# Kernel tuning notes

Hardware: AMD Instinct MI355X
Metric: run time of the kernel (lower is better)

Reference implementation:

```python
import jax, jax.numpy as jnp
import numpy as np

B = 32768      # batch size
D = 256        # embedding dim
C = 2048       # number of classes (label range)
WEIGHT = 1.0
TEMPERATURE = 0.3
EPS = 1e-12


def setup_inputs() -> dict:
    key = jax.random.key(0)
    k1, k2 = jax.random.split(key)
    features = jax.random.normal(k1, (B, D), dtype=jnp.float32)
    labels = jax.random.randint(k2, (B,), 0, C, dtype=jnp.int32)
    return {"features": features, "labels": labels, "epoch": 5}


def reference(features, labels, epoch):
    # L2-normalize embeddings (F.normalize, p=2, dim=1)
    norms = jnp.sqrt(jnp.sum(features * features, axis=1, keepdims=True))
    f = features / jnp.maximum(norms, EPS)                      # [B, D]

    # per-class segment sums / counts (vectorized replacement of the python loop)
    ones = jnp.ones((f.shape[0],), dtype=f.dtype)
    counts = jax.ops.segment_sum(ones, labels, num_segments=C)  # [C]
    sums = jax.ops.segment_sum(f, labels, num_segments=C)       # [C, D]
    centroids = sums / jnp.maximum(counts, 1.0)[:, None]        # [C, D] (mean; empty classes masked later)

    # leave-one-out positive centroid: (sum_class - f_i) / (n_class - 1)
    cnt_i = counts[labels]                                       # [B]
    c_p = (sums[labels] - f) / jnp.maximum(cnt_i - 1.0, 1.0)[:, None]
    d_p = jnp.sqrt(jnp.sum((f - c_p) ** 2, axis=1) + EPS)        # [B]

    # distances to all class centroids: ||f||=1 after normalization
    cn2 = jnp.sum(centroids * centroids, axis=1)                 # [C]
    d2 = 1.0 + cn2[None, :] - 2.0 * (f @ centroids.T)           # [B, C]
    d = jnp.sqrt(jnp.maximum(d2, EPS))

    # mask own class and empty (absent-in-batch) classes, take min negative distance
    class_ids = jnp.arange(C, dtype=labels.dtype)
    neg_mask = (counts[None, :] > 0) & (labels[:, None] != class_ids[None, :])
    d_n = jnp.min(jnp.where(neg_mask, d, jnp.inf), axis=1)       # [B]

    # samples are skipped if their class is a singleton or no negative class exists
    valid = (cnt_i > 1.0) & jnp.isfinite(d_n)
    d_n_safe = jnp.where(jnp.isfinite(d_n), d_n, 0.0)

    # temperature schedule: min(temperature + 0.02*epoch, 1)
    temp = min(TEMPERATURE + 0.02 * epoch, 1.0)

    # ln(1 + exp((d_p - d_n)/t)) == softplus
    loss_per_sample = jax.nn.softplus((d_p - d_n_safe) / temp)
    cnt = jnp.sum(valid.astype(f.dtype))
    loss = jnp.where(cnt > 0,
                     jnp.sum(jnp.where(valid, loss_per_sample, 0.0)) / jnp.maximum(cnt, 1.0),
                     0.0)
    return WEIGHT * loss
```

## Files before the change

### kernel.cpp

```cpp
#include <hip/hip_runtime.h>
#include <hip/hip_bf16.h>
#include <math.h>

constexpr int Bn = 32768;
constexpr int Dn = 256;
constexpr int Cn = 2048;
constexpr int NSPLIT = 4;
constexpr int CLS_PER_BLK = Cn / NSPLIT;
constexpr int TCLS = 32;
constexpr int NIT = CLS_PER_BLK / TCLS;
#define EPSF 1e-12f
#define INFF __builtin_inff()

typedef __bf16 bf16x8 __attribute__((ext_vector_type(8)));
typedef __bf16 bf16x4 __attribute__((ext_vector_type(4)));
typedef float  f32x4  __attribute__((ext_vector_type(4)));

__device__ inline void async_copy16(const void* g, void* l) {
    __builtin_amdgcn_global_load_lds(
        (const __attribute__((address_space(1))) void*)g,
        (__attribute__((address_space(3))) void*)l, 16, 0, 0);
}

__global__ __launch_bounds__(256) void k_prep(const float* __restrict__ feat,
                                              const int* __restrict__ labels,
                                              __bf16* __restrict__ fneg,
                                              int* __restrict__ hist) {
    const int wave = threadIdx.x >> 6, lane = threadIdx.x & 63;
    const int s = blockIdx.x * 4 + wave;
    const float4 v = ((const float4*)(feat + (size_t)s * Dn))[lane];
    float ss = v.x * v.x + v.y * v.y + v.z * v.z + v.w * v.w;
    #pragma unroll
    for (int off = 1; off < 64; off <<= 1) ss += __shfl_xor(ss, off, 64);
    const float inv = -2.0f / fmaxf(sqrtf(ss), EPSF);
    bf16x4 bf;
    bf[0] = (__bf16)(v.x * inv); bf[1] = (__bf16)(v.y * inv);
    bf[2] = (__bf16)(v.z * inv); bf[3] = (__bf16)(v.w * inv);
    *(bf16x4*)(fneg + (size_t)s * Dn + lane * 4) = bf;
    if (lane == 0) atomicAdd(&hist[labels[s]], 1);
}

__global__ __launch_bounds__(256) void k_scan(const int* __restrict__ hist,
                                              int* __restrict__ cnt_i,
                                              int* __restrict__ offs,
                                              int* __restrict__ offs_work) {
    __shared__ int part[256];
    const int t = threadIdx.x;
    int h[8], pre[8]; int sum = 0;
    #pragma unroll
    for (int j = 0; j < 8; ++j) { h[j] = hist[t * 8 + j]; pre[j] = sum; sum += h[j]; }
    int v = sum;
    part[t] = v; __syncthreads();
    for (int off = 1; off < 256; off <<= 1) {
        int add = (t >= off) ? part[t - off] : 0;
        __syncthreads();
        v += add; part[t] = v;
        __syncthreads();
    }
    const int base = v - sum;
    #pragma unroll
    for (int j = 0; j < 8; ++j) {
        const int b = t * 8 + j, o = base + pre[j];
        cnt_i[b] = h[j]; offs[b] = o; offs_work[b] = o;
    }
}

__global__ __launch_bounds__(256) void k_scatter(const int* __restrict__ labels,
                                                 int* __restrict__ offs_work,
                                                 int* __restrict__ order) {
    const int i = blockIdx.x * 256 + threadIdx.x;
    const int pos = atomicAdd(&offs_work[labels[i]], 1);
    order[pos] = i;
}

__global__ __launch_bounds__(256) void k_centseg(const __bf16* __restrict__ fneg,
                                                 const int* __restrict__ order,
                                                 const int* __restrict__ offs,
                                                 const int* __restrict__ cnt_i,
                                                 __bf16* __restrict__ centK,
                                                 float* __restrict__ cn2x) {
    const int wave = threadIdx.x >> 6, lane = threadIdx.x & 63;
    const int c = blockIdx.x * 4 + wave;
    const int n = cnt_i[c], start = offs[c];
    int myidx = 0;
    if (lane < n) myidx = order[start + lane];
    float sx = 0.f, sy = 0.f, sz = 0.f, sw = 0.f;
    const int nf = (n < 64) ? n : 64;
    for (int j = 0; j < nf; ++j) {
        const int idx = __shfl(myidx, j, 64);
        const bf16x4 v = *(const bf16x4*)(fneg + (size_t)idx * Dn + lane * 4);
        sx += -0.5f * (float)v[0]; sy += -0.5f * (float)v[1];
        sz += -0.5f * (float)v[2]; sw += -0.5f * (float)v[3];
    }
    for (int j = 64; j < n; ++j) {
        const int idx = order[start + j];
        const bf16x4 v = *(const bf16x4*)(fneg + (size_t)idx * Dn + lane * 4);
        sx += -0.5f * (float)v[0]; sy += -0.5f * (float)v[1];
        sz += -0.5f * (float)v[2]; sw += -0.5f * (float)v[3];
    }
    const float invn = 1.0f / fmaxf((float)n, 1.0f);
    const float cx = sx * invn, cy = sy * invn, cz = sz * invn, cw = sw * invn;
    bf16x4 cb; cb[0] = (__bf16)cx; cb[1] = (__bf16)cy; cb[2] = (__bf16)cz; cb[3] = (__bf16)cw;
    *(bf16x4*)(centK + ((size_t)(lane >> 1) * Cn + c) * 8 + (lane & 1) * 4) = cb;
    float ss = cx * cx + cy * cy + cz * cz + cw * cw;
    #pragma unroll
    for (int off = 1; off < 64; off <<= 1) ss += __shfl_xor(ss, off, 64);
    if (lane == 0) cn2x[c] = (n > 0) ? ss : INFF;
}

__global__ __launch_bounds__(256, 2) void k_main(const __bf16* __restrict__ fneg,
                                                 const int* __restrict__ labels,
                                                 const __bf16* __restrict__ centK,
                                                 const float* __restrict__ cn2x,
                                                 float* __restrict__ minval,
                                                 float* __restrict__ dotown) {
    __shared__ __align__(16) __bf16 sB[2][TCLS * Dn];
    __shared__ float s_cn2[CLS_PER_BLK];
    const int lane = threadIdx.x & 63, wave = threadIdx.x >> 6;
    const int m16 = lane & 15, quad = lane >> 4;
    const int sbase = blockIdx.x * 256 + wave * 64;
    const int c_begin = blockIdx.y * CLS_PER_BLK;

    bf16x8 a[4][8];
    #pragma unroll
    for (int p = 0; p < 4; ++p) {
        const __bf16* fr = fneg + (size_t)(sbase + p * 16 + m16) * Dn + quad * 8;
        #pragma unroll
        for (int t = 0; t < 8; ++t) a[p][t] = *(const bf16x8*)(fr + t * 32);
    }
    int lab[4][4];
    #pragma unroll
    for (int p = 0; p < 4; ++p)
        #pragma unroll
        for (int r = 0; r < 4; ++r)
            lab[p][r] = labels[sbase + p * 16 + quad * 4 + r];

    float rm[4][4], dacc[4][4];
    #pragma unroll
    for (int p = 0; p < 4; ++p)
        #pragma unroll
        for (int r = 0; r < 4; ++r) { rm[p][r] = INFF; dacc[p][r] = 0.0f; }

    auto stage = [&](int buf, int it) {
        const int c0 = c_begin + it * TCLS;
        #pragma unroll
        for (int j = 0; j < 4; ++j) {
            const int chunk = wave * 256 + j * 64 + lane;
            const int h  = chunk >> 9;
            const int kc = (chunk >> 4) & 31;
            const int n  = chunk & 15;
            const __bf16* g = centK + ((size_t)kc * Cn + (c0 + h * 16 + n)) * 8;
            __bf16* l = &sB[buf][(size_t)(wave * 256 + j * 64) * 8];
            async_copy16(g, l);
        }
    };

    stage(0, 0);
    for (int c = threadIdx.x; c < CLS_PER_BLK; c += 256) s_cn2[c] = cn2x[c_begin + c];
    __syncthreads();
    for (int it = 0; it < NIT; ++it) {
        const int cur = it & 1;
        if (it + 1 < NIT) stage(cur ^ 1, it + 1);
        #pragma unroll
        for (int hh = 0; hh < 2; ++hh) {
            const int ctile = it * TCLS + hh * 16;
            const float cn2v = s_cn2[ctile + m16];
            const __bf16* ls = &sB[cur][hh * 4096];
            f32x4 acc[4] = {{0.f,0.f,0.f,0.f},{0.f,0.f,0.f,0.f},
                            {0.f,0.f,0.f,0.f},{0.f,0.f,0.f,0.f}};
            #pragma unroll
            for (int t = 0; t < 8; ++t) {
                const bf16x8 b = *(const bf16x8*)(ls + t * 512 + lane * 8);
                #pragma unroll
                for (int p = 0; p < 4; ++p)
                    acc[p] = __builtin_amdgcn_mfma_f32_16x16x32_bf16(a[p][t], b, acc[p], 0, 0, 0);
            }
            const int crow = c_begin + ctile + m16;
            #pragma unroll
            for (int p = 0; p < 4; ++p)
                #pragma unroll
                for (int r = 0; r < 4; ++r) {
                    const bool own = (crow == lab[p][r]);
                    const float sel = own ? INFF : cn2v;
                    rm[p][r] = fminf(rm[p][r], sel + acc[p][r]);
                    dacc[p][r] += own ? acc[p][r] : 0.0f;
                }
        }
        __syncthreads();
    }
    #pragma unroll
    for (int off = 1; off < 16; off <<= 1)
        #pragma unroll
        for (int p = 0; p < 4; ++p)
            #pragma unroll
            for (int r = 0; r < 4; ++r) {
                rm[p][r] = fminf(rm[p][r], __shfl_xor(rm[p][r], off, 64));
                dacc[p][r] += __shfl_xor(dacc[p][r], off, 64);
            }
    if (m16 == 0) {
        float* mv = minval + (size_t)blockIdx.y * Bn;
        float* dv = dotown + (size_t)blockIdx.y * Bn;
        #pragma unroll
        for (int p = 0; p < 4; ++p)
            #pragma unroll
            for (int r = 0; r < 4; ++r) {
                mv[sbase + p * 16 + quad * 4 + r] = rm[p][r];
                dv[sbase + p * 16 + quad * 4 + r] = dacc[p][r];
            }
    }
}

__global__ __launch_bounds__(256) void k_final(const int* __restrict__ labels,
                                               const int* __restrict__ cnt_i,
                                               const float* __restrict__ cn2x,
                                               const float* __restrict__ minval,
                                               const float* __restrict__ dotown,
                                               const int* __restrict__ epoch,
                                               float* __restrict__ accum) {
    const int i = blockIdx.x * 256 + threadIdx.x;
    const int lane = threadIdx.x & 63;
    const float temp = fminf(0.3f + 0.02f * (float)(*epoch), 1.0f);
    float m = minval[i];
    float draw = dotown[i];
    #pragma unroll
    for (int k = 1; k < NSPLIT; ++k) {
        m = fminf(m, minval[(size_t)k * Bn + i]);
        draw += dotown[(size_t)k * Bn + i];
    }
    const int l = labels[i];
    const int n = cnt_i[l];
    const float nf = (float)n;
    const float cn2 = cn2x[l];
    const float fds = nf * (-0.5f * draw);
    const float fm1 = fmaxf(nf - 1.0f, 1.0f);
    const float fdcp = (fds - 1.0f) / fm1;
    const float cp2 = (nf * nf * cn2 - 2.0f * fds + 1.0f) / (fm1 * fm1);
    const float dp2 = 1.0f - 2.0f * fdcp + cp2;
    const float d_p = sqrtf(fmaxf(dp2, 0.0f) + EPSF);
    const bool finite = (m < 1e37f);
    const float d_n = finite ? sqrtf(fmaxf(1.0f + m, EPSF)) : 0.0f;
    const bool valid = (n > 1) && finite;
    const float x = (d_p - d_n) / temp;
    const float sp = fmaxf(x, 0.0f) + log1pf(expf(-fabsf(x)));
    float ws = valid ? sp : 0.0f, wc = valid ? 1.0f : 0.0f;
    #pragma unroll
    for (int off = 1; off < 64; off <<= 1) {
        ws += __shfl_xor(ws, off, 64);
        wc += __shfl_xor(wc, off, 64);
    }
    if (lane == 0) {
        atomicAdd(&accum[0], ws);
        atomicAdd(&accum[1], wc);
    }
}

__global__ void k_out(const float* __restrict__ accum, float* __restrict__ out) {
    const float s = accum[0], c = accum[1];
    out[0] = (c > 0.0f) ? (s / fmaxf(c, 1.0f)) : 0.0f;
}

extern "C" void kernel_launch(void* const* d_in, const int* in_sizes, int n_in,
                              void* d_out, int out_size, void* d_ws, size_t ws_size,
                              hipStream_t stream) {
    const float* feat  = (const float*)d_in[0];
    const int* labels  = (const int*)d_in[1];
    const int* epoch   = (const int*)d_in[2];
    float* out = (float*)d_out;
    char* ws = (char*)d_ws;

    size_t off = 0;
    __bf16* fneg     = (__bf16*)(ws + off); off += (size_t)Bn * Dn * 2;
    __bf16* centK    = (__bf16*)(ws + off); off += (size_t)Cn * Dn * 2;
    float*  cn2x     = (float*)(ws + off);  off += (size_t)Cn * 4;
    int*    hist     = (int*)(ws + off);    off += (size_t)Cn * 4;
    int*    cnt_i    = (int*)(ws + off);    off += (size_t)Cn * 4;
    int*    offs     = (int*)(ws + off);    off += (size_t)Cn * 4;
    int*    offs_wk  = (int*)(ws + off);    off += (size_t)Cn * 4;
    int*    order    = (int*)(ws + off);    off += (size_t)Bn * 4;
    float*  minval   = (float*)(ws + off);  off += (size_t)NSPLIT * Bn * 4;
    float*  dotown   = (float*)(ws + off);  off += (size_t)NSPLIT * Bn * 4;
    float*  accum    = (float*)(ws + off);  off += 2 * 4;

    (void)hipMemsetAsync(hist,  0, (size_t)Cn * sizeof(int), stream);
    (void)hipMemsetAsync(accum, 0, 2 * sizeof(float), stream);

    k_prep<<<Bn / 4, 256, 0, stream>>>(feat, labels, fneg, hist);
    k_scan<<<1, 256, 0, stream>>>(hist, cnt_i, offs, offs_wk);
    k_scatter<<<Bn / 256, 256, 0, stream>>>(labels, offs_wk, order);
    k_centseg<<<Cn / 4, 256, 0, stream>>>(fneg, order, offs, cnt_i, centK, cn2x);
    dim3 g5(Bn / 256, NSPLIT);
    k_main<<<g5, 256, 0, stream>>>(fneg, labels, centK, cn2x, minval, dotown);
    k_final<<<Bn / 256, 256, 0, stream>>>(labels, cnt_i, cn2x, minval, dotown,
                                          epoch, accum);
    k_out<<<1, 1, 0, stream>>>(accum, out);
}
```

Baseline: 162.5 us.

## Fuse all stages into one persistent kernel with software grid barriers

Replaces the seven separate kernel launches and two memsets with a single persistent kernel of 512 blocks. Stages are separated by an atomic-counter grid barrier, and the three zeroed buffers are laid out contiguously so one memset clears them. The aim is to remove launch gaps and per-kernel tail effects. In exchange it adds six global barriers, relies on all 512 blocks being co-resident (256 CUs times 2 blocks), and has a bounded spin guard that could silently break the barrier. Stages that used many small blocks now run on fewer blocks with more work each.

```diff
diff --git a/kernel.cpp b/kernel.cpp
--- a/kernel.cpp
+++ b/kernel.cpp
@@ -9,6 +9,7 @@
 constexpr int CLS_PER_BLK = Cn / NSPLIT;
 constexpr int TCLS = 32;
 constexpr int NIT = CLS_PER_BLK / TCLS;
+constexpr int NBLK = 512;
 #define EPSF 1e-12f
 #define INFF __builtin_inff()
 
@@ -22,241 +23,259 @@
         (__attribute__((address_space(3))) void*)l, 16, 0, 0);
 }
 
-__global__ __launch_bounds__(256) void k_prep(const float* __restrict__ feat,
-                                              const int* __restrict__ labels,
-                                              __bf16* __restrict__ fneg,
-                                              int* __restrict__ hist) {
-    const int wave = threadIdx.x >> 6, lane = threadIdx.x & 63;
-    const int s = blockIdx.x * 4 + wave;
-    const float4 v = ((const float4*)(feat + (size_t)s * Dn))[lane];
-    float ss = v.x * v.x + v.y * v.y + v.z * v.z + v.w * v.w;
-    #pragma unroll
-    for (int off = 1; off < 64; off <<= 1) ss += __shfl_xor(ss, off, 64);
-    const float inv = -2.0f / fmaxf(sqrtf(ss), EPSF);
-    bf16x4 bf;
-    bf[0] = (__bf16)(v.x * inv); bf[1] = (__bf16)(v.y * inv);
-    bf[2] = (__bf16)(v.z * inv); bf[3] = (__bf16)(v.w * inv);
-    *(bf16x4*)(fneg + (size_t)s * Dn + lane * 4) = bf;
-    if (lane == 0) atomicAdd(&hist[labels[s]], 1);
+__device__ inline void gbar(unsigned* bar, unsigned target) {
+    __syncthreads();
+    if (threadIdx.x == 0) {
+        __threadfence();
+        __hip_atomic_fetch_add(bar, 1u, __ATOMIC_RELAXED, __HIP_MEMORY_SCOPE_AGENT);
+        int guard = 0;
+        while (__hip_atomic_load(bar, __ATOMIC_RELAXED, __HIP_MEMORY_SCOPE_AGENT) < target
+               && guard < (1 << 22)) {
+            __builtin_amdgcn_s_sleep(2);
+            ++guard;
+        }
+        __threadfence();
+    }
+    __syncthreads();
 }
 
-__global__ __launch_bounds__(256) void k_scan(const int* __restrict__ hist,
-                                              int* __restrict__ cnt_i,
-                                              int* __restrict__ offs,
-                                              int* __restrict__ offs_work) {
-    __shared__ int part[256];
-    const int t = threadIdx.x;
-    int h[8], pre[8]; int sum = 0;
-    #pragma unroll
-    for (int j = 0; j < 8; ++j) { h[j] = hist[t * 8 + j]; pre[j] = sum; sum += h[j]; }
-    int v = sum;
-    part[t] = v; __syncthreads();
-    for (int off = 1; off < 256; off <<= 1) {
-        int add = (t >= off) ? part[t - off] : 0;
-        __syncthreads();
-        v += add; part[t] = v;
-        __syncthreads();
-    }
-    const int base = v - sum;
-    #pragma unroll
-    for (int j = 0; j < 8; ++j) {
-        const int b = t * 8 + j, o = base + pre[j];
-        cnt_i[b] = h[j]; offs[b] = o; offs_work[b] = o;
-    }
-}
-
-__global__ __launch_bounds__(256) void k_scatter(const int* __restrict__ labels,
-                                                 int* __restrict__ offs_work,
-                                                 int* __restrict__ order) {
-    const int i = blockIdx.x * 256 + threadIdx.x;
-    const int pos = atomicAdd(&offs_work[labels[i]], 1);
-    order[pos] = i;
-}
-
-__global__ __launch_bounds__(256) void k_centseg(const __bf16* __restrict__ fneg,
-                                                 const int* __restrict__ order,
-                                                 const int* __restrict__ offs,
-                                                 const int* __restrict__ cnt_i,
-                                                 __bf16* __restrict__ centK,
-                                                 float* __restrict__ cn2x) {
-    const int wave = threadIdx.x >> 6, lane = threadIdx.x & 63;
-    const int c = blockIdx.x * 4 + wave;
-    const int n = cnt_i[c], start = offs[c];
-    int myidx = 0;
-    if (lane < n) myidx = order[start + lane];
-    float sx = 0.f, sy = 0.f, sz = 0.f, sw = 0.f;
-    const int nf = (n < 64) ? n : 64;
-    for (int j = 0; j < nf; ++j) {
-        const int idx = __shfl(myidx, j, 64);
-        const bf16x4 v = *(const bf16x4*)(fneg + (size_t)idx * Dn + lane * 4);
-        sx += -0.5f * (float)v[0]; sy += -0.5f * (float)v[1];
-        sz += -0.5f * (float)v[2]; sw += -0.5f * (float)v[3];
-    }
-    for (int j = 64; j < n; ++j) {
-        const int idx = order[start + j];
-        const bf16x4 v = *(const bf16x4*)(fneg + (size_t)idx * Dn + lane * 4);
-        sx += -0.5f * (float)v[0]; sy += -0.5f * (float)v[1];
-        sz += -0.5f * (float)v[2]; sw += -0.5f * (float)v[3];
-    }
-    const float invn = 1.0f / fmaxf((float)n, 1.0f);
-    const float cx = sx * invn, cy = sy * invn, cz = sz * invn, cw = sw * invn;
-    bf16x4 cb; cb[0] = (__bf16)cx; cb[1] = (__bf16)cy; cb[2] = (__bf16)cz; cb[3] = (__bf16)cw;
-    *(bf16x4*)(centK + ((size_t)(lane >> 1) * Cn + c) * 8 + (lane & 1) * 4) = cb;
-    float ss = cx * cx + cy * cy + cz * cz + cw * cw;
-    #pragma unroll
-    for (int off = 1; off < 64; off <<= 1) ss += __shfl_xor(ss, off, 64);
-    if (lane == 0) cn2x[c] = (n > 0) ? ss : INFF;
-}
-
-__global__ __launch_bounds__(256, 2) void k_main(const __bf16* __restrict__ fneg,
-                                                 const int* __restrict__ labels,
-                                                 const __bf16* __restrict__ centK,
-                                                 const float* __restrict__ cn2x,
-                                                 float* __restrict__ minval,
-                                                 float* __restrict__ dotown) {
+__global__ __launch_bounds__(256, 2) void k_all(
+    const float* __restrict__ feat, const int* __restrict__ labels,
+    const int* __restrict__ epoch,
+    __bf16* __restrict__ fneg, __bf16* __restrict__ centK,
+    float* __restrict__ cn2x, int* __restrict__ hist,
+    int* __restrict__ cnt_i, int* __restrict__ offs,
+    int* __restrict__ offs_wk, int* __restrict__ order,
+    float* __restrict__ minval, float* __restrict__ dotown,
+    float* __restrict__ accum, unsigned* __restrict__ bar,
+    float* __restrict__ out)
+{
+    const int tid = threadIdx.x, bx = blockIdx.x;
+    const int lane = tid & 63, wave = tid >> 6;
+
     __shared__ __align__(16) __bf16 sB[2][TCLS * Dn];
     __shared__ float s_cn2[CLS_PER_BLK];
-    const int lane = threadIdx.x & 63, wave = threadIdx.x >> 6;
-    const int m16 = lane & 15, quad = lane >> 4;
-    const int sbase = blockIdx.x * 256 + wave * 64;
-    const int c_begin = blockIdx.y * CLS_PER_BLK;
-
-    bf16x8 a[4][8];
-    #pragma unroll
-    for (int p = 0; p < 4; ++p) {
-        const __bf16* fr = fneg + (size_t)(sbase + p * 16 + m16) * Dn + quad * 8;
-        #pragma unroll
-        for (int t = 0; t < 8; ++t) a[p][t] = *(const bf16x8*)(fr + t * 32);
-    }
-    int lab[4][4];
-    #pragma unroll
-    for (int p = 0; p < 4; ++p)
-        #pragma unroll
-        for (int r = 0; r < 4; ++r)
-            lab[p][r] = labels[sbase + p * 16 + quad * 4 + r];
-
-    float rm[4][4], dacc[4][4];
-    #pragma unroll
-    for (int p = 0; p < 4; ++p)
-        #pragma unroll
-        for (int r = 0; r < 4; ++r) { rm[p][r] = INFF; dacc[p][r] = 0.0f; }
-
-    auto stage = [&](int buf, int it) {
-        const int c0 = c_begin + it * TCLS;
-        #pragma unroll
-        for (int j = 0; j < 4; ++j) {
-            const int chunk = wave * 256 + j * 64 + lane;
-            const int h  = chunk >> 9;
-            const int kc = (chunk >> 4) & 31;
-            const int n  = chunk & 15;
-            const __bf16* g = centK + ((size_t)kc * Cn + (c0 + h * 16 + n)) * 8;
-            __bf16* l = &sB[buf][(size_t)(wave * 256 + j * 64) * 8];
-            async_copy16(g, l);
-        }
-    };
-
-    stage(0, 0);
-    for (int c = threadIdx.x; c < CLS_PER_BLK; c += 256) s_cn2[c] = cn2x[c_begin + c];
-    __syncthreads();
-    for (int it = 0; it < NIT; ++it) {
-        const int cur = it & 1;
-        if (it + 1 < NIT) stage(cur ^ 1, it + 1);
-        #pragma unroll
-        for (int hh = 0; hh < 2; ++hh) {
-            const int ctile = it * TCLS + hh * 16;
-            const float cn2v = s_cn2[ctile + m16];
-            const __bf16* ls = &sB[cur][hh * 4096];
-            f32x4 acc[4] = {{0.f,0.f,0.f,0.f},{0.f,0.f,0.f,0.f},
-                            {0.f,0.f,0.f,0.f},{0.f,0.f,0.f,0.f}};
-            #pragma unroll
-            for (int t = 0; t < 8; ++t) {
-                const bf16x8 b = *(const bf16x8*)(ls + t * 512 + lane * 8);
+
+    {
+        #pragma unroll 4
+        for (int w = 0; w < 16; ++w) {
+            const int s = bx * 64 + w * 4 + wave;
+            const float4 v = ((const float4*)(feat + (size_t)s * Dn))[lane];
+            float ss = v.x * v.x + v.y * v.y + v.z * v.z + v.w * v.w;
+            #pragma unroll
+            for (int off = 1; off < 64; off <<= 1) ss += __shfl_xor(ss, off, 64);
+            const float inv = -2.0f / fmaxf(sqrtf(ss), EPSF);
+            bf16x4 bf;
+            bf[0] = (__bf16)(v.x * inv); bf[1] = (__bf16)(v.y * inv);
+            bf[2] = (__bf16)(v.z * inv); bf[3] = (__bf16)(v.w * inv);
+            *(bf16x4*)(fneg + (size_t)s * Dn + lane * 4) = bf;
+            if (lane == 0) atomicAdd(&hist[labels[s]], 1);
+        }
+    }
+    gbar(bar, 1u * NBLK);
+
+    if (bx == 0) {
+        int* part = (int*)s_cn2;
+        int h[8], pre[8]; int sum = 0;
+        #pragma unroll
+        for (int j = 0; j < 8; ++j) { h[j] = hist[tid * 8 + j]; pre[j] = sum; sum += h[j]; }
+        int v = sum;
+        part[tid] = v; __syncthreads();
+        for (int off = 1; off < 256; off <<= 1) {
+            int add = (tid >= off) ? part[tid - off] : 0;
+            __syncthreads();
+            v += add; part[tid] = v;
+            __syncthreads();
+        }
+        const int base = v - sum;
+        #pragma unroll
+        for (int j = 0; j < 8; ++j) {
+            const int b = tid * 8 + j, o = base + pre[j];
+            cnt_i[b] = h[j]; offs[b] = o; offs_wk[b] = o;
+        }
+    }
+    gbar(bar, 2u * NBLK);
+
+    {
+        const int i = bx * 256 + tid;
+        if (i < Bn) {
+            const int pos = atomicAdd(&offs_wk[labels[i]], 1);
+            order[pos] = i;
+        }
+    }
+    gbar(bar, 3u * NBLK);
+
+    {
+        const int c = bx * 4 + wave;
+        const int n = cnt_i[c], start = offs[c];
+        int myidx = 0;
+        if (lane < n) myidx = order[start + lane];
+        float sx = 0.f, sy = 0.f, sz = 0.f, sw = 0.f;
+        const int nf = (n < 64) ? n : 64;
+        for (int j = 0; j < nf; ++j) {
+            const int idx = __shfl(myidx, j, 64);
+            const bf16x4 v = *(const bf16x4*)(fneg + (size_t)idx * Dn + lane * 4);
+            sx += -0.5f * (float)v[0]; sy += -0.5f * (float)v[1];
+            sz += -0.5f * (float)v[2]; sw += -0.5f * (float)v[3];
+        }
+        for (int j = 64; j < n; ++j) {
+            const int idx = order[start + j];
+            const bf16x4 v = *(const bf16x4*)(fneg + (size_t)idx * Dn + lane * 4);
+            sx += -0.5f * (float)v[0]; sy += -0.5f * (float)v[1];
+            sz += -0.5f * (float)v[2]; sw += -0.5f * (float)v[3];
+        }
+        const float invn = 1.0f / fmaxf((float)n, 1.0f);
+        const float cx = sx * invn, cy = sy * invn, cz = sz * invn, cw = sw * invn;
+        bf16x4 cb; cb[0] = (__bf16)cx; cb[1] = (__bf16)cy;
+        cb[2] = (__bf16)cz; cb[3] = (__bf16)cw;
+        *(bf16x4*)(centK + ((size_t)(lane >> 1) * Cn + c) * 8 + (lane & 1) * 4) = cb;
+        float ss = cx * cx + cy * cy + cz * cz + cw * cw;
+        #pragma unroll
+        for (int off = 1; off < 64; off <<= 1) ss += __shfl_xor(ss, off, 64);
+        if (lane == 0) cn2x[c] = (n > 0) ? ss : INFF;
+    }
+    gbar(bar, 4u * NBLK);
+
+    {
+        const int bxm = bx & 127, split = bx >> 7;
+        const int m16 = lane & 15, quad = lane >> 4;
+        const int sbase = bxm * 256 + wave * 64;
+        const int c_begin = split * CLS_PER_BLK;
+
+        bf16x8 a[4][8];
+        #pragma unroll
+        for (int p = 0; p < 4; ++p) {
+            const __bf16* fr = fneg + (size_t)(sbase + p * 16 + m16) * Dn + quad * 8;
+            #pragma unroll
+            for (int t = 0; t < 8; ++t) a[p][t] = *(const bf16x8*)(fr + t * 32);
+        }
+        int lab[4][4];
+        #pragma unroll
+        for (int p = 0; p < 4; ++p)
+            #pragma unroll
+            for (int r = 0; r < 4; ++r)
+                lab[p][r] = labels[sbase + p * 16 + quad * 4 + r];
+
+        float rm[4][4], dacc[4][4];
+        #pragma unroll
+        for (int p = 0; p < 4; ++p)
+            #pragma unroll
+            for (int r = 0; r < 4; ++r) { rm[p][r] = INFF; dacc[p][r] = 0.0f; }
+
+        auto stage = [&](int buf, int it) {
+            const int c0 = c_begin + it * TCLS;
+            #pragma unroll
+            for (int j = 0; j < 4; ++j) {
+                const int chunk = wave * 256 + j * 64 + lane;
+                const int h  = chunk >> 9;
+                const int kc = (chunk >> 4) & 31;
+                const int n  = chunk & 15;
+                const __bf16* g = centK + ((size_t)kc * Cn + (c0 + h * 16 + n)) * 8;
+                __bf16* l = &sB[buf][(size_t)(wave * 256 + j * 64) * 8];
+                async_copy16(g, l);
+            }
+        };
+
+        stage(0, 0);
+        for (int c = tid; c < CLS_PER_BLK; c += 256) s_cn2[c] = cn2x[c_begin + c];
+        __syncthreads();
+        for (int it = 0; it < NIT; ++it) {
+            const int cur = it & 1;
+            if (it + 1 < NIT) stage(cur ^ 1, it + 1);
+            #pragma unroll
+            for (int hh = 0; hh < 2; ++hh) {
+                const int ctile = it * TCLS + hh * 16;
+                const float cn2v = s_cn2[ctile + m16];
+                const __bf16* ls = &sB[cur][hh * 4096];
+                f32x4 acc[4] = {{0.f,0.f,0.f,0.f},{0.f,0.f,0.f,0.f},
+                                {0.f,0.f,0.f,0.f},{0.f,0.f,0.f,0.f}};
+                #pragma unroll
+                for (int t = 0; t < 8; ++t) {
+                    const bf16x8 b = *(const bf16x8*)(ls + t * 512 + lane * 8);
+                    #pragma unroll
+                    for (int p = 0; p < 4; ++p)
+                        acc[p] = __builtin_amdgcn_mfma_f32_16x16x32_bf16(a[p][t], b, acc[p], 0, 0, 0);
+                }
+                const int crow = c_begin + ctile + m16;
                 #pragma unroll
                 for (int p = 0; p < 4; ++p)
-                    acc[p] = __builtin_amdgcn_mfma_f32_16x16x32_bf16(a[p][t], b, acc[p], 0, 0, 0);
-            }
-            const int crow = c_begin + ctile + m16;
+                    #pragma unroll
+                    for (int r = 0; r < 4; ++r) {
+                        const bool own = (crow == lab[p][r]);
+                        const float sel = own ? INFF : cn2v;
+                        rm[p][r] = fminf(rm[p][r], sel + acc[p][r]);
+                        dacc[p][r] += own ? acc[p][r] : 0.0f;
+                    }
+            }
+            __syncthreads();
+        }
+        #pragma unroll
+        for (int off = 1; off < 16; off <<= 1)
             #pragma unroll
             for (int p = 0; p < 4; ++p)
                 #pragma unroll
                 for (int r = 0; r < 4; ++r) {
-                    const bool own = (crow == lab[p][r]);
-                    const float sel = own ? INFF : cn2v;
-                    rm[p][r] = fminf(rm[p][r], sel + acc[p][r]);
-                    dacc[p][r] += own ? acc[p][r] : 0.0f;
+                    rm[p][r] = fminf(rm[p][r], __shfl_xor(rm[p][r], off, 64));
+                    dacc[p][r] += __shfl_xor(dacc[p][r], off, 64);
                 }
-        }
-        __syncthreads();
-    }
-    #pragma unroll
-    for (int off = 1; off < 16; off <<= 1)
-        #pragma unroll
-        for (int p = 0; p < 4; ++p)
-            #pragma unroll
-            for (int r = 0; r < 4; ++r) {
-                rm[p][r] = fminf(rm[p][r], __shfl_xor(rm[p][r], off, 64));
-                dacc[p][r] += __shfl_xor(dacc[p][r], off, 64);
-            }
-    if (m16 == 0) {
-        float* mv = minval + (size_t)blockIdx.y * Bn;
-        float* dv = dotown + (size_t)blockIdx.y * Bn;
-        #pragma unroll
-        for (int p = 0; p < 4; ++p)
-            #pragma unroll
-            for (int r = 0; r < 4; ++r) {
-                mv[sbase + p * 16 + quad * 4 + r] = rm[p][r];
-                dv[sbase + p * 16 + quad * 4 + r] = dacc[p][r];
-            }
-    }
-}
-
-__global__ __launch_bounds__(256) void k_final(const int* __restrict__ labels,
-                                               const int* __restrict__ cnt_i,
-                                               const float* __restrict__ cn2x,
-                                               const float* __restrict__ minval,
-                                               const float* __restrict__ dotown,
-                                               const int* __restrict__ epoch,
-                                               float* __restrict__ accum) {
-    const int i = blockIdx.x * 256 + threadIdx.x;
-    const int lane = threadIdx.x & 63;
-    const float temp = fminf(0.3f + 0.02f * (float)(*epoch), 1.0f);
-    float m = minval[i];
-    float draw = dotown[i];
-    #pragma unroll
-    for (int k = 1; k < NSPLIT; ++k) {
-        m = fminf(m, minval[(size_t)k * Bn + i]);
-        draw += dotown[(size_t)k * Bn + i];
-    }
-    const int l = labels[i];
-    const int n = cnt_i[l];
-    const float nf = (float)n;
-    const float cn2 = cn2x[l];
-    const float fds = nf * (-0.5f * draw);
-    const float fm1 = fmaxf(nf - 1.0f, 1.0f);
-    const float fdcp = (fds - 1.0f) / fm1;
-    const float cp2 = (nf * nf * cn2 - 2.0f * fds + 1.0f) / (fm1 * fm1);
-    const float dp2 = 1.0f - 2.0f * fdcp + cp2;
-    const float d_p = sqrtf(fmaxf(dp2, 0.0f) + EPSF);
-    const bool finite = (m < 1e37f);
-    const float d_n = finite ? sqrtf(fmaxf(1.0f + m, EPSF)) : 0.0f;
-    const bool valid = (n > 1) && finite;
-    const float x = (d_p - d_n) / temp;
-    const float sp = fmaxf(x, 0.0f) + log1pf(expf(-fabsf(x)));
-    float ws = valid ? sp : 0.0f, wc = valid ? 1.0f : 0.0f;
-    #pragma unroll
-    for (int off = 1; off < 64; off <<= 1) {
-        ws += __shfl_xor(ws, off, 64);
-        wc += __shfl_xor(wc, off, 64);
-    }
-    if (lane == 0) {
-        atomicAdd(&accum[0], ws);
-        atomicAdd(&accum[1], wc);
-    }
-}
-
-__global__ void k_out(const float* __restrict__ accum, float* __restrict__ out) {
-    const float s = accum[0], c = accum[1];
-    out[0] = (c > 0.0f) ? (s / fmaxf(c, 1.0f)) : 0.0f;
+        if (m16 == 0) {
+            float* mv = minval + (size_t)split * Bn;
+            float* dv = dotown + (size_t)split * Bn;
+            #pragma unroll
+            for (int p = 0; p < 4; ++p)
+                #pragma unroll
+                for (int r = 0; r < 4; ++r) {
+                    mv[sbase + p * 16 + quad * 4 + r] = rm[p][r];
+                    dv[sbase + p * 16 + quad * 4 + r] = dacc[p][r];
+                }
+        }
+    }
+    gbar(bar, 5u * NBLK);
+
+    {
+        const int i = bx * 256 + tid;
+        if (i < Bn) {
+            const float temp = fminf(0.3f + 0.02f * (float)(*epoch), 1.0f);
+            float m = minval[i];
+            float draw = dotown[i];
+            #pragma unroll
+            for (int k = 1; k < NSPLIT; ++k) {
+                m = fminf(m, minval[(size_t)k * Bn + i]);
+                draw += dotown[(size_t)k * Bn + i];
+            }
+            const int l = labels[i];
+            const int n = cnt_i[l];
+            const float nf = (float)n;
+            const float cn2 = cn2x[l];
+            const float fds = nf * (-0.5f * draw);
+            const float fm1 = fmaxf(nf - 1.0f, 1.0f);
+            const float fdcp = (fds - 1.0f) / fm1;
+            const float cp2 = (nf * nf * cn2 - 2.0f * fds + 1.0f) / (fm1 * fm1);
+            const float dp2 = 1.0f - 2.0f * fdcp + cp2;
+            const float d_p = sqrtf(fmaxf(dp2, 0.0f) + EPSF);
+            const bool finite = (m < 1e37f);
+            const float d_n = finite ? sqrtf(fmaxf(1.0f + m, EPSF)) : 0.0f;
+            const bool valid = (n > 1) && finite;
+            const float x = (d_p - d_n) / temp;
+            const float sp = fmaxf(x, 0.0f) + log1pf(expf(-fabsf(x)));
+            float ws = valid ? sp : 0.0f, wc = valid ? 1.0f : 0.0f;
+            #pragma unroll
+            for (int off = 1; off < 64; off <<= 1) {
+                ws += __shfl_xor(ws, off, 64);
+                wc += __shfl_xor(wc, off, 64);
+            }
+            if (lane == 0) {
+                atomicAdd(&accum[0], ws);
+                atomicAdd(&accum[1], wc);
+            }
+        }
+    }
+    gbar(bar, 6u * NBLK);
+
+    if (bx == 0 && tid == 0) {
+        const float s = accum[0], c = accum[1];
+        out[0] = (c > 0.0f) ? (s / fmaxf(c, 1.0f)) : 0.0f;
+    }
 }
 
 extern "C" void kernel_launch(void* const* d_in, const int* in_sizes, int n_in,
@@ -272,25 +291,20 @@
     __bf16* fneg     = (__bf16*)(ws + off); off += (size_t)Bn * Dn * 2;
     __bf16* centK    = (__bf16*)(ws + off); off += (size_t)Cn * Dn * 2;
     float*  cn2x     = (float*)(ws + off);  off += (size_t)Cn * 4;
-    int*    hist     = (int*)(ws + off);    off += (size_t)Cn * 4;
+    int*      hist   = (int*)(ws + off);    off += (size_t)Cn * 4;
+    float*    accum  = (float*)(ws + off);  off += 2 * 4;
+    unsigned* bar    = (unsigned*)(ws + off); off += 4;
     int*    cnt_i    = (int*)(ws + off);    off += (size_t)Cn * 4;
     int*    offs     = (int*)(ws + off);    off += (size_t)Cn * 4;
     int*    offs_wk  = (int*)(ws + off);    off += (size_t)Cn * 4;
     int*    order    = (int*)(ws + off);    off += (size_t)Bn * 4;
     float*  minval   = (float*)(ws + off);  off += (size_t)NSPLIT * Bn * 4;
     float*  dotown   = (float*)(ws + off);  off += (size_t)NSPLIT * Bn * 4;
-    float*  accum    = (float*)(ws + off);  off += 2 * 4;
-
-    (void)hipMemsetAsync(hist,  0, (size_t)Cn * sizeof(int), stream);
-    (void)hipMemsetAsync(accum, 0, 2 * sizeof(float), stream);
-
-    k_prep<<<Bn / 4, 256, 0, stream>>>(feat, labels, fneg, hist);
-    k_scan<<<1, 256, 0, stream>>>(hist, cnt_i, offs, offs_wk);
-    k_scatter<<<Bn / 256, 256, 0, stream>>>(labels, offs_wk, order);
-    k_centseg<<<Cn / 4, 256, 0, stream>>>(fneg, order, offs, cnt_i, centK, cn2x);
-    dim3 g5(Bn / 256, NSPLIT);
-    k_main<<<g5, 256, 0, stream>>>(fneg, labels, centK, cn2x, minval, dotown);
-    k_final<<<Bn / 256, 256, 0, stream>>>(labels, cnt_i, cn2x, minval, dotown,
-                                          epoch, accum);
-    k_out<<<1, 1, 0, stream>>>(accum, out);
+
+    (void)hipMemsetAsync(hist, 0, (size_t)Cn * 4 + 2 * 4 + 4, stream);
+
+    k_all<<<NBLK, 256, 0, stream>>>(feat, labels, epoch,
+                                    fneg, centK, cn2x, hist,
+                                    cnt_i, offs, offs_wk, order,
+                                    minval, dotown, accum, bar, out);
 }
```

Measured after the change: 419.2 us. +158.0%, slower.

## Fuse histogram, scan and scatter into one block; fold output into final kernel

Applied to the files above, without the earlier changes.

Moves the label histogram out of the prep kernel into a single-block kernel that builds the histogram in shared memory, scans it and scatters sample indices using shared-memory atomics. The two memsets and the separate scatter and output kernels are removed. The final reduction now uses a last-block-done counter to write the loss. This cuts launch count and global atomics, but the single block must serially process all 32K labels, which could become a longer serial stage.

```diff
diff --git a/kernel.cpp b/kernel.cpp
--- a/kernel.cpp
+++ b/kernel.cpp
@@ -23,9 +23,7 @@
 }
 
 __global__ __launch_bounds__(256) void k_prep(const float* __restrict__ feat,
-                                              const int* __restrict__ labels,
-                                              __bf16* __restrict__ fneg,
-                                              int* __restrict__ hist) {
+                                              __bf16* __restrict__ fneg) {
     const int wave = threadIdx.x >> 6, lane = threadIdx.x & 63;
     const int s = blockIdx.x * 4 + wave;
     const float4 v = ((const float4*)(feat + (size_t)s * Dn))[lane];
@@ -37,18 +35,30 @@
     bf[0] = (__bf16)(v.x * inv); bf[1] = (__bf16)(v.y * inv);
     bf[2] = (__bf16)(v.z * inv); bf[3] = (__bf16)(v.w * inv);
     *(bf16x4*)(fneg + (size_t)s * Dn + lane * 4) = bf;
-    if (lane == 0) atomicAdd(&hist[labels[s]], 1);
-}
-
-__global__ __launch_bounds__(256) void k_scan(const int* __restrict__ hist,
+}
+
+__global__ __launch_bounds__(256) void k_sort(const int* __restrict__ labels,
                                               int* __restrict__ cnt_i,
                                               int* __restrict__ offs,
-                                              int* __restrict__ offs_work) {
+                                              int* __restrict__ order,
+                                              float* __restrict__ accum,
+                                              unsigned* __restrict__ donecnt) {
+    __shared__ int sh_hist[Cn];
     __shared__ int part[256];
     const int t = threadIdx.x;
+    for (int b = t; b < Cn; b += 256) sh_hist[b] = 0;
+    if (t == 0) { accum[0] = 0.f; accum[1] = 0.f; *donecnt = 0u; }
+    __syncthreads();
+    const int4* lab4 = (const int4*)labels;
+    for (int i = t; i < Bn / 4; i += 256) {
+        const int4 l4 = lab4[i];
+        atomicAdd(&sh_hist[l4.x], 1); atomicAdd(&sh_hist[l4.y], 1);
+        atomicAdd(&sh_hist[l4.z], 1); atomicAdd(&sh_hist[l4.w], 1);
+    }
+    __syncthreads();
     int h[8], pre[8]; int sum = 0;
     #pragma unroll
-    for (int j = 0; j < 8; ++j) { h[j] = hist[t * 8 + j]; pre[j] = sum; sum += h[j]; }
+    for (int j = 0; j < 8; ++j) { h[j] = sh_hist[t * 8 + j]; pre[j] = sum; sum += h[j]; }
     int v = sum;
     part[t] = v; __syncthreads();
     for (int off = 1; off < 256; off <<= 1) {
@@ -61,16 +71,14 @@
     #pragma unroll
     for (int j = 0; j < 8; ++j) {
         const int b = t * 8 + j, o = base + pre[j];
-        cnt_i[b] = h[j]; offs[b] = o; offs_work[b] = o;
-    }
-}
-
-__global__ __launch_bounds__(256) void k_scatter(const int* __restrict__ labels,
-                                                 int* __restrict__ offs_work,
-                                                 int* __restrict__ order) {
-    const int i = blockIdx.x * 256 + threadIdx.x;
-    const int pos = atomicAdd(&offs_work[labels[i]], 1);
-    order[pos] = i;
+        cnt_i[b] = h[j]; offs[b] = o; sh_hist[b] = o;
+    }
+    __syncthreads();
+    for (int i = t; i < Bn; i += 256) {
+        const int l = labels[i];
+        const int pos = atomicAdd(&sh_hist[l], 1);
+        order[pos] = i;
+    }
 }
 
 __global__ __launch_bounds__(256) void k_centseg(const __bf16* __restrict__ fneg,
@@ -216,7 +224,9 @@
                                                const float* __restrict__ minval,
                                                const float* __restrict__ dotown,
                                                const int* __restrict__ epoch,
-                                               float* __restrict__ accum) {
+                                               float* __restrict__ accum,
+                                               unsigned* __restrict__ donecnt,
+                                               float* __restrict__ out) {
     const int i = blockIdx.x * 256 + threadIdx.x;
     const int lane = threadIdx.x & 63;
     const float temp = fminf(0.3f + 0.02f * (float)(*epoch), 1.0f);
@@ -251,12 +261,20 @@
     if (lane == 0) {
         atomicAdd(&accum[0], ws);
         atomicAdd(&accum[1], wc);
-    }
-}
-
-__global__ void k_out(const float* __restrict__ accum, float* __restrict__ out) {
-    const float s = accum[0], c = accum[1];
-    out[0] = (c > 0.0f) ? (s / fmaxf(c, 1.0f)) : 0.0f;
+        __threadfence();
+    }
+    __syncthreads();
+    if (threadIdx.x == 0) {
+        const unsigned old = atomicAdd(donecnt, 1u);
+        if (old == (unsigned)(gridDim.x - 1)) {
+            __threadfence();
+            const float s = __hip_atomic_load(&accum[0], __ATOMIC_RELAXED,
+                                              __HIP_MEMORY_SCOPE_AGENT);
+            const float c = __hip_atomic_load(&accum[1], __ATOMIC_RELAXED,
+                                              __HIP_MEMORY_SCOPE_AGENT);
+            out[0] = (c > 0.0f) ? (s / fmaxf(c, 1.0f)) : 0.0f;
+        }
+    }
 }
 
 extern "C" void kernel_launch(void* const* d_in, const int* in_sizes, int n_in,
@@ -272,25 +290,19 @@
     __bf16* fneg     = (__bf16*)(ws + off); off += (size_t)Bn * Dn * 2;
     __bf16* centK    = (__bf16*)(ws + off); off += (size_t)Cn * Dn * 2;
     float*  cn2x     = (float*)(ws + off);  off += (size_t)Cn * 4;
-    int*    hist     = (int*)(ws + off);    off += (size_t)Cn * 4;
     int*    cnt_i    = (int*)(ws + off);    off += (size_t)Cn * 4;
     int*    offs     = (int*)(ws + off);    off += (size_t)Cn * 4;
-    int*    offs_wk  = (int*)(ws + off);    off += (size_t)Cn * 4;
     int*    order    = (int*)(ws + off);    off += (size_t)Bn * 4;
     float*  minval   = (float*)(ws + off);  off += (size_t)NSPLIT * Bn * 4;
     float*  dotown   = (float*)(ws + off);  off += (size_t)NSPLIT * Bn * 4;
     float*  accum    = (float*)(ws + off);  off += 2 * 4;
-
-    (void)hipMemsetAsync(hist,  0, (size_t)Cn * sizeof(int), stream);
-    (void)hipMemsetAsync(accum, 0, 2 * sizeof(float), stream);
-
-    k_prep<<<Bn / 4, 256, 0, stream>>>(feat, labels, fneg, hist);
-    k_scan<<<1, 256, 0, stream>>>(hist, cnt_i, offs, offs_wk);
-    k_scatter<<<Bn / 256, 256, 0, stream>>>(labels, offs_wk, order);
+    unsigned* donecnt = (unsigned*)(ws + off); off += 4;
+
+    k_prep<<<Bn / 4, 256, 0, stream>>>(feat, fneg);
+    k_sort<<<1, 256, 0, stream>>>(labels, cnt_i, offs, order, accum, donecnt);
     k_centseg<<<Cn / 4, 256, 0, stream>>>(fneg, order, offs, cnt_i, centK, cn2x);
     dim3 g5(Bn / 256, NSPLIT);
     k_main<<<g5, 256, 0, stream>>>(fneg, labels, centK, cn2x, minval, dotown);
     k_final<<<Bn / 256, 256, 0, stream>>>(labels, cnt_i, cn2x, minval, dotown,
-                                          epoch, accum);
-    k_out<<<1, 1, 0, stream>>>(accum, out);
-}
+                                          epoch, accum, donecnt, out);
+}
```

Result: slower. 198.2 us (+22.0%).
